# Kernel tuning notes

Hardware: AMD Instinct MI355X
Metric: run time of the kernel (lower is better)

Reference implementation:

```python
import jax, jax.numpy as jnp
import numpy as np

N, D, F, H, DH, R = 50000, 16, 256, 8, 32, 20
HOP_NUM, TOP_K, ALPHA, NEG_SLOPE = 10, 5, 0.1, 0.2
FF_HID = 4 * F


def _ln(x, g, b, eps=1e-5):
    m = x.mean(-1, keepdims=True)
    v = ((x - m) ** 2).mean(-1, keepdims=True)
    return (x - m) / jnp.sqrt(v + eps) * g + b


def setup_inputs() -> dict:
    key = jax.random.key(0)
    ks = jax.random.split(key, 16)
    s = 0.02
    inp = {
        'ent_feat': jax.random.normal(ks[0], (N, F), jnp.float32),
        'rel_feat': jax.random.normal(ks[1], (R, F), jnp.float32),
        'W_head': jax.random.normal(ks[2], (F, H * DH), jnp.float32) * s,
        'W_tail': jax.random.normal(ks[3], (F, H * DH), jnp.float32) * s,
        'W_ent': jax.random.normal(ks[4], (F, H * DH), jnp.float32) * s,
        'W_rel': jax.random.normal(ks[5], (F, H * DH), jnp.float32) * s,
        'attn_h': jax.random.normal(ks[6], (H, DH), jnp.float32) * s,
        'attn_t': jax.random.normal(ks[7], (H, DH), jnp.float32) * s,
        'attn_r': jax.random.normal(ks[8], (H, DH), jnp.float32) * s,
        'ln_ent_g': jnp.ones((F,), jnp.float32), 'ln_ent_b': jnp.zeros((F,), jnp.float32),
        'ln_rel_g': jnp.ones((F,), jnp.float32), 'ln_rel_b': jnp.zeros((F,), jnp.float32),
        'ln_ff_g': jnp.ones((F,), jnp.float32), 'ln_ff_b': jnp.zeros((F,), jnp.float32),
        'ffn_W1': jax.random.normal(ks[9], (F, FF_HID), jnp.float32) * s,
        'ffn_b1': jnp.zeros((FF_HID,), jnp.float32),
        'ffn_W2': jax.random.normal(ks[10], (FF_HID, F), jnp.float32) * s,
        'ffn_b2': jnp.zeros((F,), jnp.float32),
        'src': jax.random.randint(ks[11], (N, D), 0, N, jnp.int32),
        'rid': jax.random.randint(ks[12], (N, D), 0, R, jnp.int32),
    }
    return inp


def reference(ent_feat, rel_feat, W_head, W_tail, W_ent, W_rel,
              attn_h, attn_t, attn_r,
              ln_ent_g, ln_ent_b, ln_rel_g, ln_rel_b, ln_ff_g, ln_ff_b,
              ffn_W1, ffn_b1, ffn_W2, ffn_b2, src, rid):
    # --- projections (dropout = 0 at eval) ---
    x = _ln(ent_feat, ln_ent_g, ln_ent_b)                    # [N,F]
    fh = (x @ W_head).reshape(N, H, DH)
    ftl = (x @ W_tail).reshape(N, H, DH)
    fe = (x @ W_ent).reshape(N, H, DH)                       # 'ft' messages
    r = _ln(rel_feat, ln_rel_g, ln_rel_b)
    fr = (r @ W_rel).reshape(R, H, DH)
    # --- per-node / per-relation attention logits ---
    eh = (fh * attn_h).sum(-1)                               # [N,H]
    et = (ftl * attn_t).sum(-1)                              # [N,H]
    er = (fr * attn_r).sum(-1)                               # [R,H]
    # edges: row i = incoming edges of dst node i, sources src[i,:]
    e = eh[src] + et[:, None, :] + er[rid]                   # [N,D,H]
    e = jnp.where(e > 0, e, NEG_SLOPE * e)                   # LeakyReLU
    # --- edge_softmax over incoming edges of each dst node ---
    a = jax.nn.softmax(e, axis=1)                            # [N,D,H]
    # --- top-k sparsification + renormalization ---
    a_t = a.transpose(0, 2, 1)                               # [N,H,D]
    topv, _ = jax.lax.top_k(a_t, TOP_K)                      # [N,H,K]
    kth = topv[..., TOP_K - 1]                               # [N,H]
    top_sum = topv.sum(-1)                                   # [N,H]
    a_n = jnp.where(a_t >= kth[..., None], a_t, 0.0) / top_sum[..., None]  # [N,H,D]
    # --- PPR diffusion: feat <- (1-a) * A @ feat + a * feat0 ---
    feat0 = fe

    def step(feat, _):
        m = feat[src]                                        # [N,D,H,DH]
        agg = jnp.einsum('ndhk,nhd->nhk', m, a_n)            # [N,H,DH]
        return (1.0 - ALPHA) * agg + ALPHA * feat0, None

    feat, _ = jax.lax.scan(step, feat0, None, length=HOP_NUM)
    # --- residual (Identity since in==out) + FFN block ---
    rst = feat + ent_feat.reshape(N, H, DH)
    rst = rst.reshape(N, F)
    y = _ln(rst, ln_ff_g, ln_ff_b)
    ff = jax.nn.relu(y @ ffn_W1 + ffn_b1) @ ffn_W2 + ffn_b2
    return ff + rst
```

## Files before the change

kernel.cpp:

```cpp
#include <hip/hip_runtime.h>

#define NN   50000
#define DD   16
#define FFE  256
#define HH   8
#define DHH  32
#define RR   20
#define HOPN 10

typedef unsigned short u16;
typedef unsigned int   u32;
typedef __attribute__((ext_vector_type(8))) short  short8;
typedef __attribute__((ext_vector_type(4))) float  floatx4;
typedef __attribute__((ext_vector_type(4))) double doublex4;

__device__ __forceinline__ float b2f(u16 u){ return __uint_as_float(((u32)u)<<16); }
__device__ __forceinline__ u16 f2b(float f){
  u32 x = __float_as_uint(f);
  u32 r = (x + 0x7fffu + ((x>>16)&1u)) >> 16;
  return (u16)r;
}

__global__ __launch_bounds__(256) void castw_kernel(
    const float* __restrict__ We, const float* __restrict__ W1,
    const float* __restrict__ W2,
    u16* __restrict__ Wet, u16* __restrict__ W1t, u16* __restrict__ W2t)
{
  int tid = blockIdx.x*256 + threadIdx.x;
  if (tid < 256*256) {
    int k = tid >> 8, n = tid & 255;
    Wet[n*256 + k] = f2b(We[tid]);
  } else if (tid < 256*256 + 256*1024) {
    int s = tid - 65536;
    int k = s >> 10, n = s & 1023;
    W1t[n*256 + k] = f2b(W1[s]);
  } else if (tid < 589824) {
    int s = tid - 327680;
    int k = s >> 8, n = s & 255;
    W2t[n*1024 + k] = f2b(W2[s]);
  }
}

__global__ __launch_bounds__(256) void prep_kernel(
    const float* __restrict__ rel_feat,
    const float* __restrict__ W_head, const float* __restrict__ W_tail,
    const float* __restrict__ W_rel,
    const float* __restrict__ attn_h, const float* __restrict__ attn_t,
    const float* __restrict__ attn_r,
    const float* __restrict__ lng, const float* __restrict__ lnb,
    double* __restrict__ Wcomb, double* __restrict__ er)
{
  int t = threadIdx.x;
  if (blockIdx.x == RR) {
    for (int h = 0; h < HH; h++) {
      double sh = 0.0, st = 0.0;
      #pragma unroll
      for (int c = 0; c < DHH; c++) {
        int j = h*DHH + c;
        sh += (double)W_head[t*FFE + j] * (double)attn_h[j];
        st += (double)W_tail[t*FFE + j] * (double)attn_t[j];
      }
      Wcomb[t*16 + h]     = sh;
      Wcomb[t*16 + 8 + h] = st;
    }
    return;
  }
  int r = blockIdx.x;
  __shared__ double red[8];
  __shared__ double rln[256];
  double v = (double)rel_feat[r*FFE + t];
  double s = v, q = v*v;
  #pragma unroll
  for (int o = 32; o; o >>= 1) { s += __shfl_xor(s, o, 64); q += __shfl_xor(q, o, 64); }
  if ((t & 63) == 0) { red[t>>6] = s; red[4 + (t>>6)] = q; }
  __syncthreads();
  double stot = red[0]+red[1]+red[2]+red[3];
  double qtot = red[4]+red[5]+red[6]+red[7];
  double mean = stot * (1.0/256.0);
  double var  = qtot * (1.0/256.0) - mean*mean;
  double rstd = 1.0 / sqrt(var + 1e-5);
  rln[t] = (v - mean) * rstd * (double)lng[t] + (double)lnb[t];
  __syncthreads();
  double acc = 0.0;
  for (int k = 0; k < 256; k++) acc += rln[k] * (double)W_rel[k*FFE + t];
  double p = acc * (double)attn_r[t];
  #pragma unroll
  for (int o = 16; o; o >>= 1) p += __shfl_down(p, o, 32);
  if ((t & 31) == 0) er[r*HH + (t>>5)] = p;
}

__global__ __launch_bounds__(256) void logits_kernel(
    const float* __restrict__ ent,
    const float* __restrict__ lng, const float* __restrict__ lnb,
    const double* __restrict__ Wcomb,
    u16* __restrict__ xb, double* __restrict__ eh, double* __restrict__ et)
{
  __shared__ double xs[16][257];
  int tid = threadIdx.x;
  int i0 = blockIdx.x * 16;
  int wave = tid >> 6, lane = tid & 63;
  for (int m = wave; m < 16; m += 4) {
    int row = i0 + m;
    float4 u = *(const float4*)&ent[row*FFE + lane*4];
    double v0 = u.x, v1 = u.y, v2 = u.z, v3 = u.w;
    double s = v0+v1+v2+v3;
    double q = v0*v0 + v1*v1 + v2*v2 + v3*v3;
    #pragma unroll
    for (int o = 32; o; o >>= 1) { s += __shfl_xor(s, o, 64); q += __shfl_xor(q, o, 64); }
    double mean = s * (1.0/256.0);
    double var  = q * (1.0/256.0) - mean*mean;
    double rstd = 1.0 / sqrt(var + 1e-5);
    float4 ug = *(const float4*)&lng[lane*4];
    float4 ub = *(const float4*)&lnb[lane*4];
    double y0 = (v0-mean)*rstd*(double)ug.x + (double)ub.x;
    double y1 = (v1-mean)*rstd*(double)ug.y + (double)ub.y;
    double y2 = (v2-mean)*rstd*(double)ug.z + (double)ub.z;
    double y3 = (v3-mean)*rstd*(double)ug.w + (double)ub.w;
    int c = lane*4;
    xs[m][c] = y0; xs[m][c+1] = y1; xs[m][c+2] = y2; xs[m][c+3] = y3;
    ushort4 o4;
    o4.x = f2b((float)y0); o4.y = f2b((float)y1);
    o4.z = f2b((float)y2); o4.w = f2b((float)y3);
    *(ushort4*)&xb[row*FFE + c] = o4;
  }
  __syncthreads();
  int nl = lane & 15, kg = lane >> 4;
  doublex4 c4 = {0.0, 0.0, 0.0, 0.0};
  #pragma unroll
  for (int kk = 0; kk < 16; kk++) {
    int k = wave*64 + kk*4 + kg;
    double a = xs[nl][k];
    double b = Wcomb[k*16 + nl];
    c4 = __builtin_amdgcn_mfma_f64_16x16x4f64(a, b, c4, 0, 0, 0);
  }
  __syncthreads();
  double* sp = &xs[0][0];
  #pragma unroll
  for (int i = 0; i < 4; i++)
    sp[wave*256 + (kg*4 + i)*16 + nl] = c4[i];
  __syncthreads();
  int m = tid >> 4, n = tid & 15;
  double v = sp[tid] + sp[256 + tid] + sp[512 + tid] + sp[768 + tid];
  if (n < 8) eh[(i0+m)*HH + n] = v;
  else       et[(i0+m)*HH + (n-8)] = v;
}

template<int EPI>
__global__ __launch_bounds__(256) void gemm_kernel(
    const u16* __restrict__ A, const u16* __restrict__ B,
    const float* __restrict__ bias,
    const u16* __restrict__ feat, const float* __restrict__ ent,
    u16* __restrict__ Obf, float* __restrict__ Of,
    int M, int N, int K)
{
  __shared__ u16 As[128][40];
  __shared__ u16 Bs[128][40];
  int t = threadIdx.x;
  int i0 = blockIdx.x * 128;
  int n0 = blockIdx.y * 128;
  int w = t >> 6, l = t & 63;
  int cr = t >> 2;
  int cc = (t & 3) * 8;
  int ga0 = min(i0 + cr, M-1);
  int ga1 = min(i0 + cr + 64, M-1);
  int gb0 = n0 + cr;
  int gb1 = n0 + cr + 64;
  floatx4 acc[2][8];
  #pragma unroll
  for (int mt = 0; mt < 2; mt++)
    #pragma unroll
    for (int nt = 0; nt < 8; nt++) acc[mt][nt] = (floatx4){0.f,0.f,0.f,0.f};
  int ln = l & 15, lq = (l >> 4) * 8;
  for (int k0 = 0; k0 < K; k0 += 32) {
    __syncthreads();
    *(uint4*)&As[cr][cc]      = *(const uint4*)&A[(size_t)ga0*K + k0 + cc];
    *(uint4*)&As[cr+64][cc]   = *(const uint4*)&A[(size_t)ga1*K + k0 + cc];
    *(uint4*)&Bs[cr][cc]      = *(const uint4*)&B[(size_t)gb0*K + k0 + cc];
    *(uint4*)&Bs[cr+64][cc]   = *(const uint4*)&B[(size_t)gb1*K + k0 + cc];
    __syncthreads();
    short8 bfr[8];
    #pragma unroll
    for (int nt = 0; nt < 8; nt++) bfr[nt] = *(const short8*)&Bs[nt*16 + ln][lq];
    #pragma unroll
    for (int mt = 0; mt < 2; mt++) {
      short8 afr = *(const short8*)&As[w*32 + mt*16 + ln][lq];
      #pragma unroll
      for (int nt = 0; nt < 8; nt++)
        acc[mt][nt] = __builtin_amdgcn_mfma_f32_16x16x32_bf16(afr, bfr[nt], acc[mt][nt], 0, 0, 0);
    }
  }
  int lr = (l >> 4) * 4;
  #pragma unroll
  for (int mt = 0; mt < 2; mt++) {
    #pragma unroll
    for (int nt = 0; nt < 8; nt++) {
      int col = n0 + nt*16 + ln;
      #pragma unroll
      for (int r = 0; r < 4; r++) {
        int row = i0 + w*32 + mt*16 + lr + r;
        if (row < M) {
          float v = acc[mt][nt][r];
          if (EPI == 0) {
            Obf[(size_t)row*N + col] = f2b(v);
          } else if (EPI == 1) {
            v += bias[col];
            Obf[(size_t)row*N + col] = f2b(v > 0.f ? v : 0.f);
          } else {
            v += bias[col] + b2f(feat[(size_t)row*FFE + col]) + ent[(size_t)row*FFE + col];
            Of[(size_t)row*N + col] = v;
          }
        }
      }
    }
  }
}

__global__ __launch_bounds__(256) void edge_kernel(
    const int* __restrict__ src, const int* __restrict__ rid,
    const double* __restrict__ eh, const double* __restrict__ et,
    const double* __restrict__ er,
    int* __restrict__ idx6, float* __restrict__ w6)
{
  int tid = blockIdx.x*256 + threadIdx.x;
  if (tid >= NN*HH) return;
  int i = tid >> 3, h = tid & 7;
  double bet = et[tid];
  double e[16]; int sj[16];
  #pragma unroll
  for (int d = 0; d < 16; d++) {
    int s = src[i*DD + d];
    int rv = rid[i*DD + d];
    sj[d] = s;
    double v = eh[s*HH + h] + bet + er[rv*HH + h];
    e[d] = (v > 0.0) ? v : 0.2 * v;
  }
  u32 mask = 0; double vs[5]; int js[5];
  #pragma unroll
  for (int k = 0; k < 5; k++) {
    double best = -1e300; int bj = 0, bd = 0;
    #pragma unroll
    for (int d = 0; d < 16; d++) {
      bool c = (((mask>>d)&1u) == 0u) && (e[d] > best);
      if (c) { best = e[d]; bj = sj[d]; bd = d; }
    }
    mask |= (1u << bd); vs[k] = best; js[k] = bj;
  }
  double kth = vs[4];
  int j6 = 0; bool f6 = false;
  #pragma unroll
  for (int d = 0; d < 16; d++) {
    if ((((mask>>d)&1u) == 0u) && (e[d] == kth) && !f6) { j6 = sj[d]; f6 = true; }
  }
  float m0 = (float)vs[0];
  float ex[5], ssum = 0.f;
  #pragma unroll
  for (int k = 0; k < 5; k++) { ex[k] = __expf((float)vs[k] - m0); ssum += ex[k]; }
  float inv = 0.9f / ssum;
  long base = (long)tid * 6;
  #pragma unroll
  for (int k = 0; k < 5; k++) { idx6[base+k] = js[k]; w6[base+k] = ex[k]*inv; }
  idx6[base+5] = j6; w6[base+5] = f6 ? ex[4]*inv : 0.f;
}

__global__ __launch_bounds__(256) void diff_kernel(
    const u16* __restrict__ fold, const u16* __restrict__ fe,
    const int* __restrict__ idx6, const float* __restrict__ w6,
    u16* __restrict__ fnew)
{
  int i = blockIdx.x, tid = threadIdx.x;
  int h = tid >> 5, c = tid & 31;
  long eb = ((long)i*HH + h) * 6;
  float acc = 0.1f * b2f(fe[i*FFE + tid]);
  #pragma unroll
  for (int k = 0; k < 5; k++) {
    int j = idx6[eb + k];
    float w = w6[eb + k];
    acc += w * b2f(fold[(size_t)j*FFE + h*DHH + c]);
  }
  float w5 = w6[eb + 5];
  if (w5 != 0.f) {
    int j = idx6[eb + 5];
    acc += w5 * b2f(fold[(size_t)j*FFE + h*DHH + c]);
  }
  fnew[i*FFE + tid] = f2b(acc);
}

__global__ __launch_bounds__(256) void ln_ff_kernel(
    const u16* __restrict__ feat, const float* __restrict__ ent,
    const float* __restrict__ g, const float* __restrict__ b,
    u16* __restrict__ y)
{
  int w = threadIdx.x >> 6, l = threadIdx.x & 63;
  int row = blockIdx.x*4 + w;
  float4 e4 = *(const float4*)&ent[row*FFE + l*4];
  ushort4 fv = *(const ushort4*)&feat[row*FFE + l*4];
  float v0 = b2f(fv.x)+e4.x, v1 = b2f(fv.y)+e4.y;
  float v2 = b2f(fv.z)+e4.z, v3 = b2f(fv.w)+e4.w;
  float s = v0+v1+v2+v3;
  float q = v0*v0 + v1*v1 + v2*v2 + v3*v3;
  #pragma unroll
  for (int o = 32; o; o >>= 1) { s += __shfl_xor(s, o, 64); q += __shfl_xor(q, o, 64); }
  float mean = s * (1.f/256.f);
  float var  = q * (1.f/256.f) - mean*mean;
  float rstd = rsqrtf(var + 1e-5f);
  float4 g4 = *(const float4*)&g[l*4];
  float4 b4 = *(const float4*)&b[l*4];
  ushort4 o4;
  o4.x = f2b((v0-mean)*rstd*g4.x + b4.x);
  o4.y = f2b((v1-mean)*rstd*g4.y + b4.y);
  o4.z = f2b((v2-mean)*rstd*g4.z + b4.z);
  o4.w = f2b((v3-mean)*rstd*g4.w + b4.w);
  *(ushort4*)&y[row*FFE + l*4] = o4;
}

extern "C" void kernel_launch(void* const* d_in, const int* in_sizes, int n_in,
                              void* d_out, int out_size, void* d_ws, size_t ws_size,
                              hipStream_t stream)
{
  const float* ent      = (const float*)d_in[0];
  const float* rel      = (const float*)d_in[1];
  const float* W_head   = (const float*)d_in[2];
  const float* W_tail   = (const float*)d_in[3];
  const float* W_ent    = (const float*)d_in[4];
  const float* W_rel    = (const float*)d_in[5];
  const float* attn_h   = (const float*)d_in[6];
  const float* attn_t   = (const float*)d_in[7];
  const float* attn_r   = (const float*)d_in[8];
  const float* ln_ent_g = (const float*)d_in[9];
  const float* ln_ent_b = (const float*)d_in[10];
  const float* ln_rel_g = (const float*)d_in[11];
  const float* ln_rel_b = (const float*)d_in[12];
  const float* ln_ff_g  = (const float*)d_in[13];
  const float* ln_ff_b  = (const float*)d_in[14];
  const float* W1       = (const float*)d_in[15];
  const float* b1       = (const float*)d_in[16];
  const float* W2       = (const float*)d_in[17];
  const float* b2       = (const float*)d_in[18];
  const int* src        = (const int*)d_in[19];
  const int* rid        = (const int*)d_in[20];
  float* out = (float*)d_out;

  char* w = (char*)d_ws;
  double* er64  = (double*)(w + 0);
  double* Wcomb = (double*)(w + 4096);
  double* eh64 = (double*)(w + 36864);
  double* et64 = (double*)(w + 3236864);
  u16*    xb   = (u16*)  (w + 6436864);
  u16*    fe   = (u16*)  (w + 32036864);
  u16*    fA   = (u16*)  (w + 57636864);
  int*    idx6 = (int*)  (w + 83236864);
  float*  w6   = (float*)(w + 92836864);
  u16*    h1   = (u16*)  (w + 0);
  u16*    fB   = (u16*)  (w + 102436864);
  u16*    y    = (u16*)  (w + 128036864);
  u16*    Wet  = (u16*)  (w + 153636864);
  u16*    W1t  = (u16*)  (w + 153767936);
  u16*    W2t  = (u16*)  (w + 154292224);

  castw_kernel<<<2304, 256, 0, stream>>>(W_ent, W1, W2, Wet, W1t, W2t);
  prep_kernel<<<RR+1, 256, 0, stream>>>(rel, W_head, W_tail, W_rel,
                                        attn_h, attn_t, attn_r,
                                        ln_rel_g, ln_rel_b, Wcomb, er64);
  logits_kernel<<<NN/16, 256, 0, stream>>>(ent, ln_ent_g, ln_ent_b, Wcomb,
                                           xb, eh64, et64);
  {
    dim3 g((NN + 127)/128, 2);
    gemm_kernel<0><<<g, 256, 0, stream>>>(xb, Wet, nullptr, nullptr, nullptr,
                                          fe, nullptr, NN, 256, 256);
  }
  edge_kernel<<<(NN*HH + 255)/256, 256, 0, stream>>>(src, rid, eh64, et64, er64,
                                                     idx6, w6);
  const u16* cur = fe;
  u16* bufs[2] = { fA, fB };
  for (int hop = 0; hop < HOPN; hop++) {
    u16* nxt = bufs[hop & 1];
    diff_kernel<<<NN, 256, 0, stream>>>(cur, fe, idx6, w6, nxt);
    cur = nxt;
  }
  ln_ff_kernel<<<NN/4, 256, 0, stream>>>(cur, ent, ln_ff_g, ln_ff_b, y);
  {
    dim3 g((NN + 127)/128, 8);
    gemm_kernel<1><<<g, 256, 0, stream>>>(y, W1t, b1, nullptr, nullptr,
                                          h1, nullptr, NN, 1024, 256);
  }
  {
    dim3 g((NN + 127)/128, 2);
    gemm_kernel<2><<<g, 256, 0, stream>>>(h1, W2t, b2, cur, ent,
                                          nullptr, out, NN, 256, 1024);
  }
}
```

Baseline: 809.2 us.

## Rewrite GEMM with direct global-to-LDS loads, XOR swizzle, and 2x2 wave tiling

The bf16 GEMM now moves tiles from global memory straight into LDS with global_load_lds instead of going through registers. It also doubles the K step to 64 and applies an XOR swizzle to the LDS layout to avoid bank conflicts. Work is split across waves as a 2x2 grid of 64x64 tiles, which cuts redundant LDS fragment reads per MFMA. The risks are correctness of the global_load_lds addressing (each wave writes contiguous 512-element chunks) and higher accumulator register pressure.

```diff
diff --git a/kernel.cpp b/kernel.cpp
--- a/kernel.cpp
+++ b/kernel.cpp
@@ -19,6 +19,12 @@
   u32 x = __float_as_uint(f);
   u32 r = (x + 0x7fffu + ((x>>16)&1u)) >> 16;
   return (u16)r;
+}
+
+__device__ __forceinline__ void glds16(const u16* g, u16* l) {
+  __builtin_amdgcn_global_load_lds(
+      (const __attribute__((address_space(1))) void*)g,
+      (__attribute__((address_space(3))) void*)l, 16, 0, 0);
 }
 
 __global__ __launch_bounds__(256) void castw_kernel(
@@ -153,51 +159,65 @@
     u16* __restrict__ Obf, float* __restrict__ Of,
     int M, int N, int K)
 {
-  __shared__ u16 As[128][40];
-  __shared__ u16 Bs[128][40];
+  __shared__ u16 As[128*64];
+  __shared__ u16 Bs[128*64];
   int t = threadIdx.x;
   int i0 = blockIdx.x * 128;
   int n0 = blockIdx.y * 128;
   int w = t >> 6, l = t & 63;
-  int cr = t >> 2;
-  int cc = (t & 3) * 8;
-  int ga0 = min(i0 + cr, M-1);
-  int ga1 = min(i0 + cr + 64, M-1);
-  int gb0 = n0 + cr;
-  int gb1 = n0 + cr + 64;
-  floatx4 acc[2][8];
-  #pragma unroll
-  for (int mt = 0; mt < 2; mt++)
-    #pragma unroll
-    for (int nt = 0; nt < 8; nt++) acc[mt][nt] = (floatx4){0.f,0.f,0.f,0.f};
-  int ln = l & 15, lq = (l >> 4) * 8;
-  for (int k0 = 0; k0 < K; k0 += 32) {
+  int wr = w >> 1, wc = w & 1;
+
+  int lrow = l >> 3;
+  int scol = ((l & 7) ^ lrow) * 8;
+
+  int ln = l & 15, q = l >> 4;
+  int colk0 = (q*8) ^ ((ln & 7) << 3);
+  int colk1 = colk0 ^ 32;
+
+  floatx4 acc[4][4];
+  #pragma unroll
+  for (int mt = 0; mt < 4; mt++)
+    #pragma unroll
+    for (int nt = 0; nt < 4; nt++) acc[mt][nt] = (floatx4){0.f,0.f,0.f,0.f};
+
+  for (int k0 = 0; k0 < K; k0 += 64) {
+    #pragma unroll
+    for (int j = 0; j < 4; j++) {
+      int ra = w*32 + j*8 + lrow;
+      int ga = min(i0 + ra, M-1);
+      glds16(&A[(size_t)ga*K + k0 + scol], &As[(w*4+j)*512]);
+      int gb = n0 + ra;
+      glds16(&B[(size_t)gb*K + k0 + scol], &Bs[(w*4+j)*512]);
+    }
     __syncthreads();
-    *(uint4*)&As[cr][cc]      = *(const uint4*)&A[(size_t)ga0*K + k0 + cc];
-    *(uint4*)&As[cr+64][cc]   = *(const uint4*)&A[(size_t)ga1*K + k0 + cc];
-    *(uint4*)&Bs[cr][cc]      = *(const uint4*)&B[(size_t)gb0*K + k0 + cc];
-    *(uint4*)&Bs[cr+64][cc]   = *(const uint4*)&B[(size_t)gb1*K + k0 + cc];
+    #pragma unroll
+    for (int ks = 0; ks < 2; ks++) {
+      int ck = ks ? colk1 : colk0;
+      short8 bfr[4], afr[4];
+      #pragma unroll
+      for (int nt = 0; nt < 4; nt++)
+        bfr[nt] = *(const short8*)&Bs[(wc*64 + nt*16 + ln)*64 + ck];
+      #pragma unroll
+      for (int mt = 0; mt < 4; mt++)
+        afr[mt] = *(const short8*)&As[(wr*64 + mt*16 + ln)*64 + ck];
+      #pragma unroll
+      for (int mt = 0; mt < 4; mt++)
+        #pragma unroll
+        for (int nt = 0; nt < 4; nt++)
+          acc[mt][nt] = __builtin_amdgcn_mfma_f32_16x16x32_bf16(afr[mt], bfr[nt], acc[mt][nt], 0, 0, 0);
+    }
     __syncthreads();
-    short8 bfr[8];
-    #pragma unroll
-    for (int nt = 0; nt < 8; nt++) bfr[nt] = *(const short8*)&Bs[nt*16 + ln][lq];
-    #pragma unroll
-    for (int mt = 0; mt < 2; mt++) {
-      short8 afr = *(const short8*)&As[w*32 + mt*16 + ln][lq];
-      #pragma unroll
-      for (int nt = 0; nt < 8; nt++)
-        acc[mt][nt] = __builtin_amdgcn_mfma_f32_16x16x32_bf16(afr, bfr[nt], acc[mt][nt], 0, 0, 0);
-    }
-  }
-  int lr = (l >> 4) * 4;
-  #pragma unroll
-  for (int mt = 0; mt < 2; mt++) {
-    #pragma unroll
-    for (int nt = 0; nt < 8; nt++) {
-      int col = n0 + nt*16 + ln;
+  }
+
+  int lr = q * 4;
+  #pragma unroll
+  for (int mt = 0; mt < 4; mt++) {
+    #pragma unroll
+    for (int nt = 0; nt < 4; nt++) {
+      int col = n0 + wc*64 + nt*16 + ln;
       #pragma unroll
       for (int r = 0; r < 4; r++) {
-        int row = i0 + w*32 + mt*16 + lr + r;
+        int row = i0 + wr*64 + mt*16 + lr + r;
         if (row < M) {
           float v = acc[mt][nt][r];
           if (EPI == 0) {
```

After: 808.4 us. About the same (-0.1%).
